# Kernel tuning notes

Measured on AMD Instinct MI355X. Metric: run time of the kernel, lower is better.

## Reference

```python
import jax, jax.numpy as jnp
import numpy as np

SCALES = (8, 16, 32)
RATIOS = (0.5, 1.0, 2.0)
STRIDE = 16
K = len(SCALES) * len(RATIOS)
PRE_NMS = 6000
POST_NMS = 2000
NMS_THRESH = 0.7
ROIS_PER_IMG = 128
FG_ROIS = 32
FG_THRESH = 0.5
BG_HI = 0.5
BG_LO = 0.1
NUM_GT = 20
BBOX_CLIP = 4.135  # log(1000/16), standard delta clamp


def _generate_anchors(image_width, image_height):
    base = float(STRIDE)
    ctr = (base - 1.0) / 2.0
    size = base * base
    ratios = np.array(RATIOS, dtype=np.float64)
    scales = np.array(SCALES, dtype=np.float64)
    ws = np.round(np.sqrt(size / ratios))
    hs = np.round(ws * ratios)
    ws = (ws[:, None] * scales[None, :]).reshape(-1)  # (K,) ratio-major
    hs = (hs[:, None] * scales[None, :]).reshape(-1)
    anchors = np.stack([ctr - 0.5 * (ws - 1), ctr - 0.5 * (hs - 1),
                        ctr + 0.5 * (ws - 1), ctr + 0.5 * (hs - 1)], axis=1)  # (K,4)
    fw = image_width // STRIDE
    fh = image_height // STRIDE
    sx = np.arange(fw) * STRIDE
    sy = np.arange(fh) * STRIDE
    sxx, syy = np.meshgrid(sx, sy)  # (fh, fw)
    shifts = np.stack([sxx.ravel(), syy.ravel(), sxx.ravel(), syy.ravel()], axis=1)  # (fh*fw,4)
    all_anchors = (shifts[:, None, :] + anchors[None, :, :]).reshape(-1, 4)  # (fh*fw*K,4), K fastest
    return jnp.asarray(all_anchors, jnp.float32)


def _conv2d(x, w, b):
    y = jax.lax.conv_general_dilated(x, w, (1, 1), 'SAME',
                                     dimension_numbers=('NHWC', 'HWIO', 'NHWC'))
    return y + b


def _bbox_transform_inv(anchors, deltas):
    w = anchors[:, 2] - anchors[:, 0] + 1.0
    h = anchors[:, 3] - anchors[:, 1] + 1.0
    cx = anchors[:, 0] + 0.5 * w
    cy = anchors[:, 1] + 0.5 * h
    dx, dy = deltas[:, 0], deltas[:, 1]
    dw = jnp.clip(deltas[:, 2], -BBOX_CLIP, BBOX_CLIP)
    dh = jnp.clip(deltas[:, 3], -BBOX_CLIP, BBOX_CLIP)
    pcx = dx * w + cx
    pcy = dy * h + cy
    pw = jnp.exp(dw) * w
    ph = jnp.exp(dh) * h
    return jnp.stack([pcx - 0.5 * pw, pcy - 0.5 * ph,
                      pcx + 0.5 * pw, pcy + 0.5 * ph], axis=1)


def _pairwise_iou(a, b):
    area_a = (a[:, 2] - a[:, 0] + 1.0) * (a[:, 3] - a[:, 1] + 1.0)
    area_b = (b[:, 2] - b[:, 0] + 1.0) * (b[:, 3] - b[:, 1] + 1.0)
    xx1 = jnp.maximum(a[:, None, 0], b[None, :, 0])
    yy1 = jnp.maximum(a[:, None, 1], b[None, :, 1])
    xx2 = jnp.minimum(a[:, None, 2], b[None, :, 2])
    yy2 = jnp.minimum(a[:, None, 3], b[None, :, 3])
    iw = jnp.clip(xx2 - xx1 + 1.0, 0.0)
    ih = jnp.clip(yy2 - yy1 + 1.0, 0.0)
    inter = iw * ih
    return inter / (area_a[:, None] + area_b[None, :] - inter)


def _nms_keep(boxes, thresh):
    # boxes assumed sorted by score descending; greedy suppression
    n = boxes.shape[0]
    iou = _pairwise_iou(boxes, boxes)  # (n, n)
    idx = jnp.arange(n)
    def body(i, keep):
        sup = (iou[i] > thresh) & (idx > i)
        return jnp.where(keep[i], keep & ~sup, keep)
    return jax.lax.fori_loop(0, n, body, jnp.ones((n,), jnp.bool_))


def _forward(inputs, w_shared, b_shared, w_cls, b_cls, w_bbox, b_bbox,
             gt_boxes, image_width, image_height):
    fh = image_height // STRIDE
    fw = image_width // STRIDE
    anchors = _generate_anchors(image_width, image_height)  # (fh*fw*K, 4)

    shared = _conv2d(inputs, w_shared, b_shared)
    rpn_cls_score = _conv2d(shared, w_cls, b_cls)      # (1, fh, fw, 2K)
    rpn_bbox_pred = _conv2d(shared, w_bbox, b_bbox)    # (1, fh, fw, 4K)

    # softmax over the 2 (bg, fg) channels per anchor
    cls_prob = jax.nn.softmax(rpn_cls_score.reshape(1, fh, fw, K, 2), axis=-1)
    fg_scores = cls_prob[..., 1].reshape(-1)           # (fh*fw*K,)
    deltas = rpn_bbox_pred.reshape(-1, 4)              # (fh*fw*K, 4)

    # ---- proposal_layer ----
    proposals = _bbox_transform_inv(anchors, deltas)
    proposals = jnp.stack([
        jnp.clip(proposals[:, 0], 0.0, image_width - 1.0),
        jnp.clip(proposals[:, 1], 0.0, image_height - 1.0),
        jnp.clip(proposals[:, 2], 0.0, image_width - 1.0),
        jnp.clip(proposals[:, 3], 0.0, image_height - 1.0)], axis=1)

    top_scores, order = jax.lax.top_k(fg_scores, PRE_NMS)
    top_boxes = proposals[order]                       # (PRE_NMS, 4), score-sorted

    keep = _nms_keep(jax.lax.stop_gradient(top_boxes), NMS_THRESH)
    n = PRE_NMS
    rank = jnp.where(keep, jnp.arange(n), n + jnp.arange(n))
    sel = jnp.argsort(rank)[:POST_NMS]                 # kept boxes first, score order
    roi_boxes = top_boxes[sel]                         # (POST_NMS, 4)
    roi_scores = top_scores[sel]
    rois = jnp.concatenate([jnp.zeros((POST_NMS, 1), roi_boxes.dtype), roi_boxes], axis=1)

    # ---- proposal_target_layer (deterministic top-k sampling) ----
    ov = _pairwise_iou(roi_boxes, gt_boxes[:, :4])     # (POST_NMS, NUM_GT)
    max_ov = ov.max(axis=1)
    fg_key = jnp.where(max_ov >= FG_THRESH, max_ov, -1.0)
    _, fg_idx = jax.lax.top_k(fg_key, FG_ROIS)
    bg_key = jnp.where((max_ov < BG_HI) & (max_ov >= BG_LO), max_ov, -1.0)
    _, bg_idx = jax.lax.top_k(bg_key, ROIS_PER_IMG - FG_ROIS)
    keep_inds = jnp.concatenate([fg_idx, bg_idx])      # (128,)
    return rois[keep_inds]                             # (128, 5)


def setup_inputs() -> dict:
    key = jax.random.key(0)
    ks = jax.random.split(key, 10)
    C_in, C_mid = 1024, 256
    inputs = jax.random.normal(ks[0], (1, 64, 64, C_in), jnp.float32)
    w_shared = jax.random.normal(ks[1], (3, 3, C_in, C_mid), jnp.float32) * np.sqrt(2.0 / (9 * C_in))
    b_shared = jnp.zeros((C_mid,), jnp.float32)
    w_cls = jax.random.normal(ks[2], (1, 1, C_mid, 2 * K), jnp.float32) * np.sqrt(2.0 / C_mid)
    b_cls = jnp.zeros((2 * K,), jnp.float32)
    w_bbox = jax.random.normal(ks[3], (1, 1, C_mid, 4 * K), jnp.float32) * (0.1 * np.sqrt(2.0 / C_mid))
    b_bbox = jnp.zeros((4 * K,), jnp.float32)
    # valid gt boxes inside a 1024x1024 image
    cx = jax.random.uniform(ks[4], (NUM_GT,), minval=100.0, maxval=900.0)
    cy = jax.random.uniform(ks[5], (NUM_GT,), minval=100.0, maxval=900.0)
    bw = jax.random.uniform(ks[6], (NUM_GT,), minval=32.0, maxval=300.0)
    bh = jax.random.uniform(ks[7], (NUM_GT,), minval=32.0, maxval=300.0)
    cls = jax.random.randint(ks[8], (NUM_GT,), 1, 21).astype(jnp.float32)
    gt_boxes = jnp.stack([jnp.clip(cx - bw / 2, 0.0, 1023.0), jnp.clip(cy - bh / 2, 0.0, 1023.0),
                          jnp.clip(cx + bw / 2, 0.0, 1023.0), jnp.clip(cy + bh / 2, 0.0, 1023.0),
                          cls], axis=1)
    return {"inputs": inputs, "w_shared": w_shared, "b_shared": b_shared,
            "w_cls": w_cls, "b_cls": b_cls, "w_bbox": w_bbox, "b_bbox": b_bbox,
            "gt_boxes": gt_boxes, "image_width": 1024, "image_height": 1024}


def reference(inputs, w_shared, b_shared, w_cls, b_cls, w_bbox, b_bbox,
              gt_boxes, image_width, image_height):
    return _forward(inputs, w_shared, b_shared, w_cls, b_cls, w_bbox, b_bbox,
                    gt_boxes, image_width, image_height)
```

## Files before the change

kernel.cpp:

```cpp
#include <hip/hip_runtime.h>
#include <cstdint>
#include <cstddef>

#define M_POS 4096
#define NCH   256
#define KTOT  9216
#define NANCH 36864
#define NSORT 65536
#define PRE   6000
#define POST  2000
#define NGRP  94
#define MROW  6016
#define NSLOT 14

typedef unsigned long long u64;
typedef unsigned int u32;

__device__ __forceinline__ u32 ord_f32(float f) {
  u32 u = __float_as_uint(f);
  return (u & 0x80000000u) ? ~u : (u | 0x80000000u);
}

__global__ __launch_bounds__(256) void conv3x3(const float* __restrict__ in,
                                               const float* __restrict__ wgt,
                                               float* __restrict__ part,
                                               int kPer) {
  __shared__ __align__(16) float As[16][128];
  __shared__ __align__(16) float Bs[16][128];
  int tid = threadIdx.x;
  int bm = blockIdx.x << 7;
  int bn = blockIdx.y << 7;
  int kBeg = blockIdx.z * kPer;
  int am = tid & 127;
  int aq = (tid >> 7) << 2;
  int gm = bm + am;
  int y = gm >> 6, x = gm & 63;
  int bkk = tid >> 5;
  int bn4 = (tid & 31) << 2;
  int ty = tid >> 4, tx = tid & 15;

  float acc[8][8];
#pragma unroll
  for (int i = 0; i < 8; ++i)
#pragma unroll
    for (int j = 0; j < 8; ++j) acc[i][j] = 0.f;

  for (int k0 = kBeg; k0 < kBeg + kPer; k0 += 16) {
#pragma unroll
    for (int p = 0; p < 2; ++p) {
      int kk = aq + (p << 3);
      int k = k0 + kk;
      int tap = k >> 10;
      int c = k & 1023;
      int iy = y + tap / 3 - 1;
      int ix = x + tap % 3 - 1;
      float4 v = make_float4(0.f, 0.f, 0.f, 0.f);
      if (iy >= 0 && iy < 64 && ix >= 0 && ix < 64)
        v = *(const float4*)(in + (size_t)((((iy << 6) + ix) << 10) + c));
      As[kk + 0][am] = v.x;
      As[kk + 1][am] = v.y;
      As[kk + 2][am] = v.z;
      As[kk + 3][am] = v.w;
    }
#pragma unroll
    for (int p = 0; p < 2; ++p) {
      int kk = bkk + (p << 3);
      *(float4*)&Bs[kk][bn4] =
          *(const float4*)(wgt + (size_t)(k0 + kk) * NCH + bn + bn4);
    }
    __syncthreads();
#pragma unroll
    for (int kk = 0; kk < 16; ++kk) {
      float4 a0 = *(const float4*)&As[kk][ty << 2];
      float4 a1 = *(const float4*)&As[kk][64 + (ty << 2)];
      float4 b0 = *(const float4*)&Bs[kk][tx << 2];
      float4 b1 = *(const float4*)&Bs[kk][64 + (tx << 2)];
      float a[8] = {a0.x, a0.y, a0.z, a0.w, a1.x, a1.y, a1.z, a1.w};
      float b[8] = {b0.x, b0.y, b0.z, b0.w, b1.x, b1.y, b1.z, b1.w};
#pragma unroll
      for (int i = 0; i < 8; ++i)
#pragma unroll
        for (int j = 0; j < 8; ++j) acc[i][j] += a[i] * b[j];
    }
    __syncthreads();
  }
  size_t ob = (size_t)blockIdx.z * ((size_t)M_POS * NCH);
#pragma unroll
  for (int i = 0; i < 8; ++i) {
    int row = bm + ((i < 4) ? ((ty << 2) + i) : (64 + (ty << 2) + i - 4));
    float4 o0 = make_float4(acc[i][0], acc[i][1], acc[i][2], acc[i][3]);
    float4 o1 = make_float4(acc[i][4], acc[i][5], acc[i][6], acc[i][7]);
    *(float4*)(part + ob + (size_t)row * NCH + bn + (tx << 2)) = o0;
    *(float4*)(part + ob + (size_t)row * NCH + bn + 64 + (tx << 2)) = o1;
  }
}

__global__ __launch_bounds__(256) void reduce_bias(const float* __restrict__ part,
                                                   const float* __restrict__ bias,
                                                   float* __restrict__ outp, int ks) {
  int idx = blockIdx.x * 256 + threadIdx.x;
  float v = 0.f;
  for (int s = 0; s < ks; ++s) v += part[(size_t)s * (M_POS * NCH) + idx];
  outp[idx] = v + bias[idx & 255];
}

__global__ __launch_bounds__(64) void conv1x1(const float* __restrict__ sh,
                                              const float* __restrict__ wc,
                                              const float* __restrict__ bc,
                                              const float* __restrict__ wb,
                                              const float* __restrict__ bb2,
                                              float* __restrict__ cls,
                                              float* __restrict__ bbox) {
  __shared__ float row[256];
  int pos = blockIdx.x;
  int tid = threadIdx.x;
  *(float4*)&row[tid * 4] = *(const float4*)(sh + (size_t)pos * 256 + tid * 4);
  __syncthreads();
  if (tid < 18) {
    float acc = bc[tid];
    for (int c = 0; c < 256; ++c) acc += row[c] * wc[c * 18 + tid];
    cls[(size_t)pos * 18 + tid] = acc;
  } else if (tid < 54) {
    int n = tid - 18;
    float acc = bb2[n];
    for (int c = 0; c < 256; ++c) acc += row[c] * wb[c * 36 + n];
    bbox[(size_t)pos * 36 + n] = acc;
  }
}

__global__ __launch_bounds__(256) void proposals_k(const float* __restrict__ cls,
                                                   const float* __restrict__ bb,
                                                   u64* __restrict__ keys,
                                                   float* __restrict__ prop) {
  int idx = blockIdx.x * 256 + threadIdx.x;
  if (idx >= NANCH) return;
  int a = idx % 9;
  int pos = idx / 9;
  int x = pos & 63, y = pos >> 6;
  float s0 = cls[(size_t)pos * 18 + 2 * a];
  float s1 = cls[(size_t)pos * 18 + 2 * a + 1];
  float mx = fmaxf(s0, s1);
  float e0 = expf(s0 - mx), e1 = expf(s1 - mx);
  float score = e1 / (e0 + e1);
  u32 u = ord_f32(score);
  keys[idx] = ((u64)u << 32) | (u64)(0xFFFFFFFFu - (u32)idx);
  const float AW[9] = {184.f, 368.f, 736.f, 128.f, 256.f, 512.f, 88.f, 176.f, 352.f};
  const float AH[9] = {96.f, 192.f, 384.f, 128.f, 256.f, 512.f, 176.f, 352.f, 704.f};
  float w = AW[a], h = AH[a];
  float cx = (float)(x * 16) + 8.0f;
  float cy = (float)(y * 16) + 8.0f;
  float dx = bb[(size_t)pos * 36 + 4 * a + 0];
  float dy = bb[(size_t)pos * 36 + 4 * a + 1];
  float dw = bb[(size_t)pos * 36 + 4 * a + 2];
  float dh = bb[(size_t)pos * 36 + 4 * a + 3];
  dw = fminf(fmaxf(dw, -4.135f), 4.135f);
  dh = fminf(fmaxf(dh, -4.135f), 4.135f);
  float pcx = dx * w + cx;
  float pcy = dy * h + cy;
  float pw = expf(dw) * w;
  float ph = expf(dh) * h;
  float x1 = pcx - 0.5f * pw, y1 = pcy - 0.5f * ph;
  float x2 = pcx + 0.5f * pw, y2 = pcy + 0.5f * ph;
  x1 = fminf(fmaxf(x1, 0.f), 1023.f);
  y1 = fminf(fmaxf(y1, 0.f), 1023.f);
  x2 = fminf(fmaxf(x2, 0.f), 1023.f);
  y2 = fminf(fmaxf(y2, 0.f), 1023.f);
  prop[(size_t)idx * 4 + 0] = x1;
  prop[(size_t)idx * 4 + 1] = y1;
  prop[(size_t)idx * 4 + 2] = x2;
  prop[(size_t)idx * 4 + 3] = y2;
}

__global__ __launch_bounds__(1024) void sort_local(u64* keys) {
  __shared__ u64 s[2048];
  int base = blockIdx.x * 2048;
  s[threadIdx.x] = keys[base + threadIdx.x];
  s[threadIdx.x + 1024] = keys[base + threadIdx.x + 1024];
  __syncthreads();
  for (int k = 2; k <= 2048; k <<= 1) {
    for (int j = k >> 1; j >= 1; j >>= 1) {
      int t = threadIdx.x;
      int i = ((t & ~(j - 1)) << 1) | (t & (j - 1));
      int p = i | j;
      bool desc = (((base + i) & k) == 0);
      u64 a = s[i], b = s[p];
      if (desc ? (a < b) : (a > b)) { s[i] = b; s[p] = a; }
      __syncthreads();
    }
  }
  keys[base + threadIdx.x] = s[threadIdx.x];
  keys[base + threadIdx.x + 1024] = s[threadIdx.x + 1024];
}

__device__ __forceinline__ void cmpswap(u64& a, u64& b, bool desc) {
  if (desc ? (a < b) : (a > b)) { u64 t = a; a = b; b = t; }
}

__global__ __launch_bounds__(256) void sort_gstep(u64* keys, int k, int j) {
  int t = blockIdx.x * 256 + threadIdx.x;
  int i = ((t & ~(j - 1)) << 1) | (t & (j - 1));
  int p = i | j;
  bool desc = ((i & k) == 0);
  u64 a = keys[i], b = keys[p];
  if (desc ? (a < b) : (a > b)) { keys[i] = b; keys[p] = a; }
}

__global__ __launch_bounds__(256) void sort_gstep2(u64* keys, int k, int j) {
  int t = blockIdx.x * 256 + threadIdx.x;
  int j2 = j >> 1;
  int a = ((t & ~(j2 - 1)) << 1) | (t & (j2 - 1));
  int i0 = ((a & ~(j - 1)) << 1) | (a & (j - 1));
  int i1 = i0 | j2, i2 = i0 | j, i3 = i0 | j | j2;
  bool desc = ((i0 & k) == 0);
  u64 v0 = keys[i0], v1 = keys[i1], v2 = keys[i2], v3 = keys[i3];
  cmpswap(v0, v2, desc);
  cmpswap(v1, v3, desc);
  cmpswap(v0, v1, desc);
  cmpswap(v2, v3, desc);
  keys[i0] = v0; keys[i1] = v1; keys[i2] = v2; keys[i3] = v3;
}

__global__ __launch_bounds__(1024) void sort_lstep(u64* keys, int k) {
  __shared__ u64 s[2048];
  int base = blockIdx.x * 2048;
  s[threadIdx.x] = keys[base + threadIdx.x];
  s[threadIdx.x + 1024] = keys[base + threadIdx.x + 1024];
  __syncthreads();
  for (int j = 1024; j >= 1; j >>= 1) {
    int t = threadIdx.x;
    int i = ((t & ~(j - 1)) << 1) | (t & (j - 1));
    int p = i | j;
    bool desc = (((base + i) & k) == 0);
    u64 a = s[i], b = s[p];
    if (desc ? (a < b) : (a > b)) { s[i] = b; s[p] = a; }
    __syncthreads();
  }
  keys[base + threadIdx.x] = s[threadIdx.x];
  keys[base + threadIdx.x + 1024] = s[threadIdx.x + 1024];
}

__global__ __launch_bounds__(256) void gather_top(const u64* __restrict__ keys,
                                                  const float4* __restrict__ prop,
                                                  float4* __restrict__ topbox) {
  int i = blockIdx.x * 256 + threadIdx.x;
  if (i >= PRE) return;
  u64 kk = keys[i];
  u32 idx = 0xFFFFFFFFu - (u32)(kk & 0xFFFFFFFFull);
  topbox[i] = prop[idx];
}

__global__ __launch_bounds__(64) void nms_mask(const float4* __restrict__ boxes,
                                               u64* __restrict__ maskT) {
  __shared__ float4 cb[64];
  int ci = blockIdx.x, ri = blockIdx.y;
  int t = threadIdx.x;
  int col = (ci << 6) + t;
  cb[t] = (col < PRE) ? boxes[col] : make_float4(0.f, 0.f, 0.f, 0.f);
  __syncthreads();
  int r = (ri << 6) + t;
  if (r >= PRE) return;
  float4 rb = boxes[r];
  float ra = (rb.z - rb.x + 1.f) * (rb.w - rb.y + 1.f);
  u64 bits = 0ull;
  for (int cc = 0; cc < 64; ++cc) {
    int j = (ci << 6) + cc;
    if (j > r && j < PRE) {
      float4 b = cb[cc];
      float ba = (b.z - b.x + 1.f) * (b.w - b.y + 1.f);
      float xx1 = fmaxf(rb.x, b.x), yy1 = fmaxf(rb.y, b.y);
      float xx2 = fminf(rb.z, b.z), yy2 = fminf(rb.w, b.w);
      float iw = fmaxf(xx2 - xx1 + 1.f, 0.f);
      float ih = fmaxf(yy2 - yy1 + 1.f, 0.f);
      float inter = iw * ih;
      float iou = inter / (ra + ba - inter);
      if (iou > 0.7f) bits |= (1ull << cc);
    }
  }
  maskT[(size_t)ci * MROW + r] = bits;
}

__global__ __launch_bounds__(512, 2) void nms_scan(const u64* __restrict__ maskT,
                                                   u64* __restrict__ keepw) {
  __shared__ u64 keepS;
  __shared__ u64 extS;
  __shared__ u32 exitS;
  const int tid = threadIdx.x;
  const int lane = tid & 63, wv = tid >> 6;

  u64 acc[NSLOT], v[NSLOT];
#pragma unroll
  for (int i = 0; i < NSLOT; ++i) { acc[i] = 0ull; v[i] = 0ull; }

  if (wv > 0) {
#pragma unroll
    for (int i = 0; i < NSLOT; ++i) {
      int gp = wv + 7 * i;
      if (gp < NGRP) v[i] = maskT[(size_t)gp * MROW + lane];
    }
  }
  u64 x = 0ull;
  if (wv == 0) x = maskT[lane];
  u32 keptTot = 0;

  for (int g = 0; g < NGRP; ++g) {
    if (wv == 0) {
      u64 cur = 0ull;
      if (g > 0) {
        u64 e = extS;
        u32 elo = __builtin_amdgcn_readfirstlane((u32)(e & 0xFFFFFFFFull));
        u32 ehi = __builtin_amdgcn_readfirstlane((u32)(e >> 32));
        cur = ((u64)ehi << 32) | (u64)elo;
      }
      u32 xlo = (u32)(x & 0xFFFFFFFFull);
      u32 xhi = (u32)(x >> 32);
      u64 keep = 0ull;
#pragma unroll
      for (int t = 0; t < 64; ++t) {
        u32 mlo = __builtin_amdgcn_readlane(xlo, t);
        u32 mhi = __builtin_amdgcn_readlane(xhi, t);
        u64 mt = ((u64)mhi << 32) | (u64)mlo;
        u64 sup = (cur >> t) & 1ull;
        u64 sel = sup - 1ull;
        keep |= (1ull << t) & sel;
        cur |= mt & sel;
      }
      if (g == NGRP - 1) keep &= (1ull << 48) - 1ull;
      keptTot += (u32)__popcll(keep);
      if (lane == 0) {
        keepS = keep;
        exitS = (keptTot >= POST) ? 1u : 0u;
        keepw[g] = keep;
      }
      if (g + 1 < NGRP) {
        int ii = ((g + 1) << 6) + lane;
        x = (ii < PRE) ? maskT[(size_t)(g + 1) * MROW + ii] : 0ull;
      }
    }
    asm volatile("s_waitcnt lgkmcnt(0)" ::: "memory");
    __builtin_amdgcn_sched_barrier(0);
    __builtin_amdgcn_s_barrier();
    __builtin_amdgcn_sched_barrier(0);
    u32 ex = exitS;
    u64 kb = keepS;
    if (ex) {
      for (int z = g + 1 + tid; z < NGRP; z += 512) keepw[z] = 0ull;
      return;
    }
    if (wv > 0) {
      u64 sel2 = ((kb >> lane) & 1ull) ? ~0ull : 0ull;
      u64 e = 0ull;
      bool own = false;
#pragma unroll
      for (int i = 0; i < NSLOT; ++i) {
        int gp = wv + 7 * i;
        if (gp < NGRP && gp > g) {
          acc[i] |= (v[i] & sel2);
          if (gp == g + 1) { e = acc[i]; own = true; }
        }
      }
      if (own) {
#pragma unroll
        for (int s = 1; s < 64; s <<= 1) e |= __shfl_xor(e, s, 64);
        if (lane == 0) extS = e;
      }
      int col = ((g + 1) << 6) + lane;
#pragma unroll
      for (int i = 0; i < NSLOT; ++i) {
        int gp = wv + 7 * i;
        if (gp < NGRP && gp > g + 1) v[i] = maskT[(size_t)gp * MROW + col];
      }
    }
    asm volatile("s_waitcnt lgkmcnt(0)" ::: "memory");
    __builtin_amdgcn_sched_barrier(0);
    __builtin_amdgcn_s_barrier();
    __builtin_amdgcn_sched_barrier(0);
  }
}

__global__ __launch_bounds__(1024) void select_rois(const u64* __restrict__ keepw,
                                                    const float4* __restrict__ topbox,
                                                    float4* __restrict__ roibox) {
  __shared__ u32 wscan[NGRP + 1];
  __shared__ u32 wc[NGRP];
  int tid = threadIdx.x;
  if (tid < NGRP) wc[tid] = (u32)__popcll(keepw[tid]);
  __syncthreads();
  if (tid == 0) {
    u32 r = 0;
    for (int g = 0; g < NGRP; ++g) { wscan[g] = r; r += wc[g]; }
    wscan[NGRP] = r;
  }
  __syncthreads();
  u32 ktot = wscan[NGRP];
  for (int i = tid; i < PRE; i += 1024) {
    int g = i >> 6, t = i & 63;
    u64 w = keepw[g];
    bool kept = (w >> t) & 1ull;
    u32 pk = wscan[g] + (u32)__popcll(w & ((1ull << t) - 1ull));
    u32 pos = kept ? pk : (ktot + (u32)i - pk);
    if (pos < POST) roibox[pos] = topbox[i];
  }
}

__device__ void bitonic2048_desc(u64* s) {
  int tid = threadIdx.x;
  for (int k = 2; k <= 2048; k <<= 1) {
    for (int j = k >> 1; j >= 1; j >>= 1) {
      int i = ((tid & ~(j - 1)) << 1) | (tid & (j - 1));
      int p = i | j;
      bool desc = ((i & k) == 0);
      u64 a = s[i], b = s[p];
      if (desc ? (a < b) : (a > b)) { s[i] = b; s[p] = a; }
      __syncthreads();
    }
  }
}

__global__ __launch_bounds__(1024) void roi_sample(const float4* __restrict__ roibox,
                                                   const float* __restrict__ gt,
                                                   float* __restrict__ out) {
  __shared__ float mov[POST];
  __shared__ u64 sk[2048];
  __shared__ float gtb[20][4];
  __shared__ int fgsel[32];
  __shared__ int bgsel[96];
  int tid = threadIdx.x;
  if (tid < 20) {
    gtb[tid][0] = gt[tid * 5 + 0];
    gtb[tid][1] = gt[tid * 5 + 1];
    gtb[tid][2] = gt[tid * 5 + 2];
    gtb[tid][3] = gt[tid * 5 + 3];
  }
  __syncthreads();
  for (int i = tid; i < POST; i += 1024) {
    float4 b = roibox[i];
    float aa = (b.z - b.x + 1.f) * (b.w - b.y + 1.f);
    float m = -3.402823466e38f;
    for (int t = 0; t < 20; ++t) {
      float gx1 = gtb[t][0], gy1 = gtb[t][1], gx2 = gtb[t][2], gy2 = gtb[t][3];
      float ga = (gx2 - gx1 + 1.f) * (gy2 - gy1 + 1.f);
      float xx1 = fmaxf(b.x, gx1), yy1 = fmaxf(b.y, gy1);
      float xx2 = fminf(b.z, gx2), yy2 = fminf(b.w, gy2);
      float iw = fmaxf(xx2 - xx1 + 1.f, 0.f);
      float ih = fmaxf(yy2 - yy1 + 1.f, 0.f);
      float inter = iw * ih;
      float iou = inter / (aa + ga - inter);
      m = fmaxf(m, iou);
    }
    mov[i] = m;
  }
  __syncthreads();
  for (int i = tid; i < 2048; i += 1024) {
    float key;
    if (i < POST) { float v = mov[i]; key = (v >= 0.5f) ? v : -1.0f; }
    else key = -2.0f;
    sk[i] = ((u64)ord_f32(key) << 32) | (u64)(2047u - (u32)i);
  }
  __syncthreads();
  bitonic2048_desc(sk);
  if (tid < 32) fgsel[tid] = (int)(2047u - (u32)(sk[tid] & 0xFFFFFFFFull));
  __syncthreads();
  for (int i = tid; i < 2048; i += 1024) {
    float key;
    if (i < POST) {
      float v = mov[i];
      key = (v < 0.5f && v >= 0.1f) ? v : -1.0f;
    } else key = -2.0f;
    sk[i] = ((u64)ord_f32(key) << 32) | (u64)(2047u - (u32)i);
  }
  __syncthreads();
  bitonic2048_desc(sk);
  if (tid < 96) bgsel[tid] = (int)(2047u - (u32)(sk[tid] & 0xFFFFFFFFull));
  __syncthreads();
  if (tid < 128) {
    int idx = (tid < 32) ? fgsel[tid] : bgsel[tid - 32];
    float4 b = roibox[idx];
    out[tid * 5 + 0] = 0.f;
    out[tid * 5 + 1] = b.x;
    out[tid * 5 + 2] = b.y;
    out[tid * 5 + 3] = b.z;
    out[tid * 5 + 4] = b.w;
  }
}

extern "C" void kernel_launch(void* const* d_in, const int* in_sizes, int n_in,
                              void* d_out, int out_size, void* d_ws, size_t ws_size,
                              hipStream_t stream) {
  const float* in   = (const float*)d_in[0];
  const float* wsh  = (const float*)d_in[1];
  const float* bsh  = (const float*)d_in[2];
  const float* wcls = (const float*)d_in[3];
  const float* bcls = (const float*)d_in[4];
  const float* wbb  = (const float*)d_in[5];
  const float* bbb  = (const float*)d_in[6];
  const float* gt   = (const float*)d_in[7];

  char* w = (char*)d_ws;
  const size_t OFF_SHARED = 0;
  const size_t OFF_CLS    = 4194304;
  const size_t OFF_BBOX   = 4489216;
  const size_t OFF_PROP   = 5226496;
  const size_t OFF_KEYS   = 0;
  const size_t OFF_TOPBOX = 524288;
  const size_t OFF_MASK   = 620288;
  const size_t OFF_KEEPW  = 5144320;
  const size_t OFF_ROIBOX = 5145088;
  const size_t OFF_PART   = 5816320;

  float* sharedb = (float*)(w + OFF_SHARED);
  float* cls     = (float*)(w + OFF_CLS);
  float* bbox    = (float*)(w + OFF_BBOX);
  float* prop    = (float*)(w + OFF_PROP);
  u64*   keys    = (u64*)(w + OFF_KEYS);
  float4* topbox = (float4*)(w + OFF_TOPBOX);
  u64*   maskT   = (u64*)(w + OFF_MASK);
  u64*   keepw   = (u64*)(w + OFF_KEEPW);
  float4* roibox = (float4*)(w + OFF_ROIBOX);
  float* out     = (float*)d_out;

  const size_t SLICE = (size_t)M_POS * NCH * 4;
  int KS = 1;
  if      (ws_size >= OFF_PART + 16 * SLICE) KS = 16;
  else if (ws_size >= OFF_PART + 8 * SLICE)  KS = 8;
  else if (ws_size >= OFF_PART + 4 * SLICE)  KS = 4;
  else if (ws_size >= OFF_PART + 2 * SLICE)  KS = 2;
  float* part = (KS > 1) ? (float*)(w + OFF_PART) : sharedb;

  conv3x3<<<dim3(32, 2, KS), 256, 0, stream>>>(in, wsh, part, KTOT / KS);
  reduce_bias<<<4096, 256, 0, stream>>>(part, bsh, sharedb, KS);
  conv1x1<<<4096, 64, 0, stream>>>(sharedb, wcls, bcls, wbb, bbb, cls, bbox);
  hipMemsetAsync(w + (size_t)NANCH * 8, 0, (size_t)(NSORT - NANCH) * 8, stream);
  proposals_k<<<144, 256, 0, stream>>>(cls, bbox, keys, prop);
  sort_local<<<32, 1024, 0, stream>>>(keys);
  for (int k = 4096; k <= NSORT; k <<= 1) {
    int j = k >> 1;
    while (j >= 4096) {
      sort_gstep2<<<64, 256, 0, stream>>>(keys, k, j);
      j >>= 2;
    }
    if (j == 2048) {
      sort_gstep<<<128, 256, 0, stream>>>(keys, k, j);
      j >>= 1;
    }
    sort_lstep<<<32, 1024, 0, stream>>>(keys, k);
  }
  gather_top<<<24, 256, 0, stream>>>(keys, (const float4*)prop, topbox);
  nms_mask<<<dim3(NGRP, NGRP), 64, 0, stream>>>(topbox, maskT);
  nms_scan<<<1, 512, 0, stream>>>(maskT, keepw);
  select_rois<<<1, 1024, 0, stream>>>(keepw, topbox, roibox);
  roi_sample<<<1, 1024, 0, stream>>>(roibox, gt, out);
}
```

Measured before the change: 579.2 us.

## Retile conv3x3, fuse global sort steps, skip lower NMS tiles, merge tail kernels

The conv3x3 block tile shrinks from 128x128 to 128x64 and the grid doubles, which gives more blocks for occupancy at the cost of loading each A tile twice. All global bitonic sub-steps for each merge stage now run in a single kernel that keeps 2^L elements in registers, replacing multiple gstep launches. nms_mask blocks below the diagonal return early, and nms_scan, select_rois and roi_sample are merged into one 512-thread kernel that holds keep words and ROI boxes in shared memory. Together these cut launch overhead and global round trips, but the fused tail runs with half as many threads per sort step.

```diff
diff --git a/kernel.cpp b/kernel.cpp
--- a/kernel.cpp
+++ b/kernel.cpp
@@ -26,24 +26,24 @@
                                                float* __restrict__ part,
                                                int kPer) {
   __shared__ __align__(16) float As[16][128];
-  __shared__ __align__(16) float Bs[16][128];
+  __shared__ __align__(16) float Bs[16][64];
   int tid = threadIdx.x;
   int bm = blockIdx.x << 7;
-  int bn = blockIdx.y << 7;
+  int bn = blockIdx.y << 6;
   int kBeg = blockIdx.z * kPer;
   int am = tid & 127;
   int aq = (tid >> 7) << 2;
   int gm = bm + am;
   int y = gm >> 6, x = gm & 63;
-  int bkk = tid >> 5;
-  int bn4 = (tid & 31) << 2;
+  int bkk = tid >> 4;
+  int bn4 = (tid & 15) << 2;
   int ty = tid >> 4, tx = tid & 15;
 
-  float acc[8][8];
+  float acc[8][4];
 #pragma unroll
   for (int i = 0; i < 8; ++i)
 #pragma unroll
-    for (int j = 0; j < 8; ++j) acc[i][j] = 0.f;
+    for (int j = 0; j < 4; ++j) acc[i][j] = 0.f;
 
   for (int k0 = kBeg; k0 < kBeg + kPer; k0 += 16) {
 #pragma unroll
@@ -62,25 +62,20 @@
       As[kk + 2][am] = v.z;
       As[kk + 3][am] = v.w;
     }
-#pragma unroll
-    for (int p = 0; p < 2; ++p) {
-      int kk = bkk + (p << 3);
-      *(float4*)&Bs[kk][bn4] =
-          *(const float4*)(wgt + (size_t)(k0 + kk) * NCH + bn + bn4);
-    }
+    *(float4*)&Bs[bkk][bn4] =
+        *(const float4*)(wgt + (size_t)(k0 + bkk) * NCH + bn + bn4);
     __syncthreads();
 #pragma unroll
     for (int kk = 0; kk < 16; ++kk) {
       float4 a0 = *(const float4*)&As[kk][ty << 2];
       float4 a1 = *(const float4*)&As[kk][64 + (ty << 2)];
       float4 b0 = *(const float4*)&Bs[kk][tx << 2];
-      float4 b1 = *(const float4*)&Bs[kk][64 + (tx << 2)];
       float a[8] = {a0.x, a0.y, a0.z, a0.w, a1.x, a1.y, a1.z, a1.w};
-      float b[8] = {b0.x, b0.y, b0.z, b0.w, b1.x, b1.y, b1.z, b1.w};
+      float b[4] = {b0.x, b0.y, b0.z, b0.w};
 #pragma unroll
       for (int i = 0; i < 8; ++i)
 #pragma unroll
-        for (int j = 0; j < 8; ++j) acc[i][j] += a[i] * b[j];
+        for (int j = 0; j < 4; ++j) acc[i][j] += a[i] * b[j];
     }
     __syncthreads();
   }
@@ -88,10 +83,8 @@
 #pragma unroll
   for (int i = 0; i < 8; ++i) {
     int row = bm + ((i < 4) ? ((ty << 2) + i) : (64 + (ty << 2) + i - 4));
-    float4 o0 = make_float4(acc[i][0], acc[i][1], acc[i][2], acc[i][3]);
-    float4 o1 = make_float4(acc[i][4], acc[i][5], acc[i][6], acc[i][7]);
-    *(float4*)(part + ob + (size_t)row * NCH + bn + (tx << 2)) = o0;
-    *(float4*)(part + ob + (size_t)row * NCH + bn + 64 + (tx << 2)) = o1;
+    float4 o = make_float4(acc[i][0], acc[i][1], acc[i][2], acc[i][3]);
+    *(float4*)(part + ob + (size_t)row * NCH + bn + (tx << 2)) = o;
   }
 }
 
@@ -196,28 +189,24 @@
   if (desc ? (a < b) : (a > b)) { u64 t = a; a = b; b = t; }
 }
 
-__global__ __launch_bounds__(256) void sort_gstep(u64* keys, int k, int j) {
+template <int L>
+__global__ __launch_bounds__(256) void gstep_n(u64* keys, int k, int j) {
+  const int jl = j >> (L - 1);
   int t = blockIdx.x * 256 + threadIdx.x;
-  int i = ((t & ~(j - 1)) << 1) | (t & (j - 1));
-  int p = i | j;
-  bool desc = ((i & k) == 0);
-  u64 a = keys[i], b = keys[p];
-  if (desc ? (a < b) : (a > b)) { keys[i] = b; keys[p] = a; }
-}
-
-__global__ __launch_bounds__(256) void sort_gstep2(u64* keys, int k, int j) {
-  int t = blockIdx.x * 256 + threadIdx.x;
-  int j2 = j >> 1;
-  int a = ((t & ~(j2 - 1)) << 1) | (t & (j2 - 1));
-  int i0 = ((a & ~(j - 1)) << 1) | (a & (j - 1));
-  int i1 = i0 | j2, i2 = i0 | j, i3 = i0 | j | j2;
-  bool desc = ((i0 & k) == 0);
-  u64 v0 = keys[i0], v1 = keys[i1], v2 = keys[i2], v3 = keys[i3];
-  cmpswap(v0, v2, desc);
-  cmpswap(v1, v3, desc);
-  cmpswap(v0, v1, desc);
-  cmpswap(v2, v3, desc);
-  keys[i0] = v0; keys[i1] = v1; keys[i2] = v2; keys[i3] = v3;
+  int base = ((t & ~(jl - 1)) << L) | (t & (jl - 1));
+  bool desc = ((base & k) == 0);
+  u64 v[1 << L];
+#pragma unroll
+  for (int m = 0; m < (1 << L); ++m) v[m] = keys[base + m * jl];
+#pragma unroll
+  for (int l = 0; l < L; ++l) {
+    int s = 1 << (L - 1 - l);
+#pragma unroll
+    for (int m = 0; m < (1 << L); ++m)
+      if ((m & s) == 0) cmpswap(v[m], v[m | s], desc);
+  }
+#pragma unroll
+  for (int m = 0; m < (1 << L); ++m) keys[base + m * jl] = v[m];
 }
 
 __global__ __launch_bounds__(1024) void sort_lstep(u64* keys, int k) {
@@ -251,8 +240,9 @@
 
 __global__ __launch_bounds__(64) void nms_mask(const float4* __restrict__ boxes,
                                                u64* __restrict__ maskT) {
+  int ci = blockIdx.x, ri = blockIdx.y;
+  if (ci < ri) return;
   __shared__ float4 cb[64];
-  int ci = blockIdx.x, ri = blockIdx.y;
   int t = threadIdx.x;
   int col = (ci << 6) + t;
   cb[t] = (col < PRE) ? boxes[col] : make_float4(0.f, 0.f, 0.f, 0.f);
@@ -279,18 +269,28 @@
   maskT[(size_t)ci * MROW + r] = bits;
 }
 
-__global__ __launch_bounds__(512, 2) void nms_scan(const u64* __restrict__ maskT,
-                                                   u64* __restrict__ keepw) {
+__global__ __launch_bounds__(512) void nms_tail(const u64* __restrict__ maskT,
+                                                const float4* __restrict__ topbox,
+                                                const float* __restrict__ gt,
+                                                float* __restrict__ out) {
+  __shared__ u64 keepL[NGRP];
   __shared__ u64 keepS;
   __shared__ u64 extS;
   __shared__ u32 exitS;
+  __shared__ float4 roibL[POST];
+  __shared__ float mov[POST];
+  __shared__ u64 sk[2048];
+  __shared__ float gtb[20][4];
+  __shared__ int fgsel[32];
+  __shared__ int bgsel[96];
+  __shared__ u32 wscan[NGRP + 1];
+
   const int tid = threadIdx.x;
   const int lane = tid & 63, wv = tid >> 6;
 
   u64 acc[NSLOT], v[NSLOT];
 #pragma unroll
   for (int i = 0; i < NSLOT; ++i) { acc[i] = 0ull; v[i] = 0ull; }
-
   if (wv > 0) {
 #pragma unroll
     for (int i = 0; i < NSLOT; ++i) {
@@ -329,7 +329,7 @@
       if (lane == 0) {
         keepS = keep;
         exitS = (keptTot >= POST) ? 1u : 0u;
-        keepw[g] = keep;
+        keepL[g] = keep;
       }
       if (g + 1 < NGRP) {
         int ii = ((g + 1) << 6) + lane;
@@ -343,8 +343,8 @@
     u32 ex = exitS;
     u64 kb = keepS;
     if (ex) {
-      for (int z = g + 1 + tid; z < NGRP; z += 512) keepw[z] = 0ull;
-      return;
+      for (int z = g + 1 + tid; z < NGRP; z += 512) keepL[z] = 0ull;
+      break;
     }
     if (wv > 0) {
       u64 sel2 = ((kb >> lane) & 1ull) ? ~0ull : 0ull;
@@ -375,56 +375,28 @@
     __builtin_amdgcn_s_barrier();
     __builtin_amdgcn_sched_barrier(0);
   }
-}
-
-__global__ __launch_bounds__(1024) void select_rois(const u64* __restrict__ keepw,
-                                                    const float4* __restrict__ topbox,
-                                                    float4* __restrict__ roibox) {
-  __shared__ u32 wscan[NGRP + 1];
-  __shared__ u32 wc[NGRP];
-  int tid = threadIdx.x;
-  if (tid < NGRP) wc[tid] = (u32)__popcll(keepw[tid]);
+
   __syncthreads();
   if (tid == 0) {
     u32 r = 0;
-    for (int g = 0; g < NGRP; ++g) { wscan[g] = r; r += wc[g]; }
+    for (int g2 = 0; g2 < NGRP; ++g2) {
+      wscan[g2] = r;
+      r += (u32)__popcll(keepL[g2]);
+    }
     wscan[NGRP] = r;
   }
   __syncthreads();
   u32 ktot = wscan[NGRP];
-  for (int i = tid; i < PRE; i += 1024) {
-    int g = i >> 6, t = i & 63;
-    u64 w = keepw[g];
-    bool kept = (w >> t) & 1ull;
-    u32 pk = wscan[g] + (u32)__popcll(w & ((1ull << t) - 1ull));
+  for (int i = tid; i < PRE; i += 512) {
+    int g2 = i >> 6, t2 = i & 63;
+    u64 wk = keepL[g2];
+    bool kept = (wk >> t2) & 1ull;
+    u32 pk = wscan[g2] + (u32)__popcll(wk & ((1ull << t2) - 1ull));
     u32 pos = kept ? pk : (ktot + (u32)i - pk);
-    if (pos < POST) roibox[pos] = topbox[i];
-  }
-}
-
-__device__ void bitonic2048_desc(u64* s) {
-  int tid = threadIdx.x;
-  for (int k = 2; k <= 2048; k <<= 1) {
-    for (int j = k >> 1; j >= 1; j >>= 1) {
-      int i = ((tid & ~(j - 1)) << 1) | (tid & (j - 1));
-      int p = i | j;
-      bool desc = ((i & k) == 0);
-      u64 a = s[i], b = s[p];
-      if (desc ? (a < b) : (a > b)) { s[i] = b; s[p] = a; }
-      __syncthreads();
-    }
-  }
-}
-
-__global__ __launch_bounds__(1024) void roi_sample(const float4* __restrict__ roibox,
-                                                   const float* __restrict__ gt,
-                                                   float* __restrict__ out) {
-  __shared__ float mov[POST];
-  __shared__ u64 sk[2048];
-  __shared__ float gtb[20][4];
-  __shared__ int fgsel[32];
-  __shared__ int bgsel[96];
-  int tid = threadIdx.x;
+    if (pos < POST) roibL[pos] = topbox[i];
+  }
+  __syncthreads();
+
   if (tid < 20) {
     gtb[tid][0] = gt[tid * 5 + 0];
     gtb[tid][1] = gt[tid * 5 + 1];
@@ -432,8 +404,8 @@
     gtb[tid][3] = gt[tid * 5 + 3];
   }
   __syncthreads();
-  for (int i = tid; i < POST; i += 1024) {
-    float4 b = roibox[i];
+  for (int i = tid; i < POST; i += 512) {
+    float4 b = roibL[i];
     float aa = (b.z - b.x + 1.f) * (b.w - b.y + 1.f);
     float m = -3.402823466e38f;
     for (int t = 0; t < 20; ++t) {
@@ -450,31 +422,57 @@
     mov[i] = m;
   }
   __syncthreads();
-  for (int i = tid; i < 2048; i += 1024) {
+  for (int i = tid; i < 2048; i += 512) {
     float key;
-    if (i < POST) { float v = mov[i]; key = (v >= 0.5f) ? v : -1.0f; }
+    if (i < POST) { float vv = mov[i]; key = (vv >= 0.5f) ? vv : -1.0f; }
     else key = -2.0f;
     sk[i] = ((u64)ord_f32(key) << 32) | (u64)(2047u - (u32)i);
   }
   __syncthreads();
-  bitonic2048_desc(sk);
+  for (int k = 2; k <= 2048; k <<= 1) {
+    for (int j = k >> 1; j >= 1; j >>= 1) {
+#pragma unroll
+      for (int q = 0; q < 2; ++q) {
+        int t = tid + (q << 9);
+        int i = ((t & ~(j - 1)) << 1) | (t & (j - 1));
+        int p = i | j;
+        bool desc = ((i & k) == 0);
+        u64 a = sk[i], b = sk[p];
+        if (desc ? (a < b) : (a > b)) { sk[i] = b; sk[p] = a; }
+      }
+      __syncthreads();
+    }
+  }
   if (tid < 32) fgsel[tid] = (int)(2047u - (u32)(sk[tid] & 0xFFFFFFFFull));
   __syncthreads();
-  for (int i = tid; i < 2048; i += 1024) {
+  for (int i = tid; i < 2048; i += 512) {
     float key;
     if (i < POST) {
-      float v = mov[i];
-      key = (v < 0.5f && v >= 0.1f) ? v : -1.0f;
+      float vv = mov[i];
+      key = (vv < 0.5f && vv >= 0.1f) ? vv : -1.0f;
     } else key = -2.0f;
     sk[i] = ((u64)ord_f32(key) << 32) | (u64)(2047u - (u32)i);
   }
   __syncthreads();
-  bitonic2048_desc(sk);
+  for (int k = 2; k <= 2048; k <<= 1) {
+    for (int j = k >> 1; j >= 1; j >>= 1) {
+#pragma unroll
+      for (int q = 0; q < 2; ++q) {
+        int t = tid + (q << 9);
+        int i = ((t & ~(j - 1)) << 1) | (t & (j - 1));
+        int p = i | j;
+        bool desc = ((i & k) == 0);
+        u64 a = sk[i], b = sk[p];
+        if (desc ? (a < b) : (a > b)) { sk[i] = b; sk[p] = a; }
+      }
+      __syncthreads();
+    }
+  }
   if (tid < 96) bgsel[tid] = (int)(2047u - (u32)(sk[tid] & 0xFFFFFFFFull));
   __syncthreads();
   if (tid < 128) {
     int idx = (tid < 32) ? fgsel[tid] : bgsel[tid - 32];
-    float4 b = roibox[idx];
+    float4 b = roibL[idx];
     out[tid * 5 + 0] = 0.f;
     out[tid * 5 + 1] = b.x;
     out[tid * 5 + 2] = b.y;
@@ -503,8 +501,6 @@
   const size_t OFF_KEYS   = 0;
   const size_t OFF_TOPBOX = 524288;
   const size_t OFF_MASK   = 620288;
-  const size_t OFF_KEEPW  = 5144320;
-  const size_t OFF_ROIBOX = 5145088;
   const size_t OFF_PART   = 5816320;
 
   float* sharedb = (float*)(w + OFF_SHARED);
@@ -514,8 +510,6 @@
   u64*   keys    = (u64*)(w + OFF_KEYS);
   float4* topbox = (float4*)(w + OFF_TOPBOX);
   u64*   maskT   = (u64*)(w + OFF_MASK);
-  u64*   keepw   = (u64*)(w + OFF_KEEPW);
-  float4* roibox = (float4*)(w + OFF_ROIBOX);
   float* out     = (float*)d_out;
 
   const size_t SLICE = (size_t)M_POS * NCH * 4;
@@ -526,27 +520,24 @@
   else if (ws_size >= OFF_PART + 2 * SLICE)  KS = 2;
   float* part = (KS > 1) ? (float*)(w + OFF_PART) : sharedb;
 
-  conv3x3<<<dim3(32, 2, KS), 256, 0, stream>>>(in, wsh, part, KTOT / KS);
+  conv3x3<<<dim3(32, 4, KS), 256, 0, stream>>>(in, wsh, part, KTOT / KS);
   reduce_bias<<<4096, 256, 0, stream>>>(part, bsh, sharedb, KS);
   conv1x1<<<4096, 64, 0, stream>>>(sharedb, wcls, bcls, wbb, bbb, cls, bbox);
   hipMemsetAsync(w + (size_t)NANCH * 8, 0, (size_t)(NSORT - NANCH) * 8, stream);
   proposals_k<<<144, 256, 0, stream>>>(cls, bbox, keys, prop);
   sort_local<<<32, 1024, 0, stream>>>(keys);
-  for (int k = 4096; k <= NSORT; k <<= 1) {
-    int j = k >> 1;
-    while (j >= 4096) {
-      sort_gstep2<<<64, 256, 0, stream>>>(keys, k, j);
-      j >>= 2;
-    }
-    if (j == 2048) {
-      sort_gstep<<<128, 256, 0, stream>>>(keys, k, j);
-      j >>= 1;
-    }
-    sort_lstep<<<32, 1024, 0, stream>>>(keys, k);
-  }
+  gstep_n<1><<<128, 256, 0, stream>>>(keys, 4096, 2048);
+  sort_lstep<<<32, 1024, 0, stream>>>(keys, 4096);
+  gstep_n<2><<<64, 256, 0, stream>>>(keys, 8192, 4096);
+  sort_lstep<<<32, 1024, 0, stream>>>(keys, 8192);
+  gstep_n<3><<<32, 256, 0, stream>>>(keys, 16384, 8192);
+  sort_lstep<<<32, 1024, 0, stream>>>(keys, 16384);
+  gstep_n<4><<<16, 256, 0, stream>>>(keys, 32768, 16384);
+  sort_lstep<<<32, 1024, 0, stream>>>(keys, 32768);
+  gstep_n<5><<<8, 256, 0, stream>>>(keys, 65536, 32768);
+  sort_lstep<<<32, 1024, 0, stream>>>(keys, 65536);
+
   gather_top<<<24, 256, 0, stream>>>(keys, (const float4*)prop, topbox);
   nms_mask<<<dim3(NGRP, NGRP), 64, 0, stream>>>(topbox, maskT);
-  nms_scan<<<1, 512, 0, stream>>>(maskT, keepw);
-  select_rois<<<1, 1024, 0, stream>>>(keepw, topbox, roibox);
-  roi_sample<<<1, 1024, 0, stream>>>(roibox, gt, out);
-}
+  nms_tail<<<1, 512, 0, stream>>>(maskT, topbox, gt, out);
+}
```

Measured after the change: 593.7 us, median of 3. 2.5% more time.
